# Kernel optimization log

Hardware: AMD Instinct MI355X
Metric: run time of the kernel (lower is better)

## Reference

```python
import jax, jax.numpy as jnp
import numpy as np

H = 16
D_MODEL = 1024
D_HID = 50  # hidden width of the 1->50->1 mask MLP


def setup_inputs() -> dict:
    key = jax.random.key(0)
    ks = jax.random.split(key, 16)
    B, S, D = 16, 768, D_MODEL
    n, nk = 512, 256  # code length n, redundancy n-k; S = n + nk
    inp = {
        "query": jax.random.normal(ks[0], (B, S, D), jnp.float32),
        "key": jax.random.normal(ks[1], (B, S, D), jnp.float32),
        "value": jax.random.normal(ks[2], (B, S, D), jnp.float32),
        "pc_matrix": jax.random.uniform(ks[3], (nk, n), jnp.float32),
        # four Linear(d_model, d_model) layers: q, k, v, out. Stored so that y = x @ W + b.
        "Wq": jax.random.normal(ks[4], (D, D), jnp.float32) * 0.02,
        "bq": jnp.zeros((D,), jnp.float32),
        "Wk": jax.random.normal(ks[5], (D, D), jnp.float32) * 0.02,
        "bk": jnp.zeros((D,), jnp.float32),
        "Wv": jax.random.normal(ks[6], (D, D), jnp.float32) * 0.02,
        "bv": jnp.zeros((D,), jnp.float32),
        "Wo": jax.random.normal(ks[7], (D, D), jnp.float32) * 0.02,
        "bo": jnp.zeros((D,), jnp.float32),
        # one_d_mapping: Linear(1,50) -> ReLU -> Linear(50,1)
        "mw1": jax.random.normal(ks[8], (1, D_HID), jnp.float32) * 0.5,
        "mb1": jax.random.normal(ks[9], (D_HID,), jnp.float32) * 0.1,
        "mw2": jax.random.normal(ks[10], (D_HID, 1), jnp.float32) * 0.5,
        "mb2": jnp.zeros((1,), jnp.float32),
    }
    return inp


def _mask_from_pc(pc, mw1, mb1, mw2, mb2):
    # pc: (nk, n). Build (S, S) block matrix, S = n + nk.
    nknk = pc @ pc.T            # (nk, nk)
    nn = pc.T @ pc              # (n, n)
    top = jnp.concatenate([nn, pc.T], axis=1)     # (n, S)
    bot = jnp.concatenate([pc, nknk], axis=1)     # (nk, S)
    M = jnp.concatenate([top, bot], axis=0)       # (S, S)
    # elementwise 1->50->1 MLP
    h = jax.nn.relu(M[..., None] * mw1[0] + mb1)  # (S, S, 50)
    out = h @ mw2 + mb2                           # (S, S, 1)
    return out[..., 0]                            # (S, S)


def reference(query, key, value, pc_matrix, Wq, bq, Wk, bk, Wv, bv, Wo, bo,
              mw1, mb1, mw2, mb2):
    B, S, D = query.shape
    dk = D // H
    q = (query @ Wq + bq).reshape(B, S, H, dk).transpose(0, 2, 1, 3)
    k = (key @ Wk + bk).reshape(B, S, H, dk).transpose(0, 2, 1, 3)
    v = (value @ Wv + bv).reshape(B, S, H, dk).transpose(0, 2, 1, 3)
    scores = jnp.einsum("bhqd,bhkd->bhqk", q, k) / jnp.sqrt(jnp.float32(dk))
    mask = _mask_from_pc(pc_matrix, mw1, mb1, mw2, mb2)  # (S, S)
    scores = scores * mask[None, None]  # multiplicative float mask
    p = jax.nn.softmax(scores, axis=-1)  # dropout is identity in eval mode
    x = jnp.einsum("bhqk,bhkd->bhqd", p, v)
    x = x.transpose(0, 2, 1, 3).reshape(B, S, D)
    return x @ Wo + bo
```

## Files before the change

kernel.cpp:

```cpp
#include <hip/hip_runtime.h>
#include <stdint.h>

typedef _Float16 f16;
typedef _Float16 f16x8 __attribute__((ext_vector_type(8)));
typedef float f32x4 __attribute__((ext_vector_type(4)));

union U4 { uint4 u; f16 h[8]; };
union U2 { uint2 u; f16 h[4]; };

#define GLOAD16(g, l)                                                         \
  __builtin_amdgcn_global_load_lds(                                           \
      (const __attribute__((address_space(1))) void*)(g),                     \
      (__attribute__((address_space(3))) void*)(l), 16, 0, 0)

__global__ __launch_bounds__(256) void k_wt(const float* __restrict__ W0,
                                            const float* __restrict__ W1,
                                            const float* __restrict__ W2,
                                            const float* __restrict__ W3,
                                            f16* __restrict__ T0, f16* __restrict__ T1,
                                            f16* __restrict__ T2, f16* __restrict__ T3) {
    __shared__ f16 tile[64 * 65];
    int z = blockIdx.z;
    const float* W = z == 0 ? W0 : z == 1 ? W1 : z == 2 ? W2 : W3;
    f16* Wt = z == 0 ? T0 : z == 1 ? T1 : z == 2 ? T2 : T3;
    int t = threadIdx.x;
    int k0 = blockIdx.x * 64, n0 = blockIdx.y * 64;
    #pragma unroll
    for (int i = 0; i < 4; i++) {
        int cid = t + i * 256;
        int row = cid >> 4, c4 = cid & 15;
        float4 v = *(const float4*)(W + (size_t)(k0 + row) * 1024 + n0 + c4 * 4);
        tile[(c4 * 4 + 0) * 65 + row] = (f16)v.x;
        tile[(c4 * 4 + 1) * 65 + row] = (f16)v.y;
        tile[(c4 * 4 + 2) * 65 + row] = (f16)v.z;
        tile[(c4 * 4 + 3) * 65 + row] = (f16)v.w;
    }
    __syncthreads();
    #pragma unroll
    for (int i = 0; i < 2; i++) {
        int cid = t + i * 256;
        int nr = cid >> 3, kc = cid & 7;
        U4 u;
        #pragma unroll
        for (int j = 0; j < 8; j++) u.h[j] = tile[nr * 65 + kc * 8 + j];
        *(uint4*)(Wt + (size_t)(n0 + nr) * 1024 + k0 + kc * 8) = u.u;
    }
}

__global__ __launch_bounds__(256) void k_cvt(const float* __restrict__ in,
                                             f16* __restrict__ out) {
    size_t id = (size_t)blockIdx.x * 256 + threadIdx.x;
    float4 a = *(const float4*)(in + id * 8);
    float4 b = *(const float4*)(in + id * 8 + 4);
    U4 u;
    u.h[0] = (f16)a.x; u.h[1] = (f16)a.y; u.h[2] = (f16)a.z; u.h[3] = (f16)a.w;
    u.h[4] = (f16)b.x; u.h[5] = (f16)b.y; u.h[6] = (f16)b.z; u.h[7] = (f16)b.w;
    *(uint4*)(out + id * 8) = u.u;
}

template <int TRANS>
__global__ __launch_bounds__(256) void k_gram(const float* __restrict__ pc,
                                              float* __restrict__ out) {
    constexpr int N = TRANS ? 256 : 512;
    constexpr int K = TRANS ? 512 : 256;
    __shared__ float As[16][68];
    __shared__ float Bs[16][68];
    int t = threadIdx.x;
    int i0 = blockIdx.x * 64, j0 = blockIdx.y * 64;
    int ty = t >> 4, tx = t & 15;
    float acc[4][4];
    #pragma unroll
    for (int r = 0; r < 4; r++)
        #pragma unroll
        for (int c = 0; c < 4; c++) acc[r][c] = 0.f;

    for (int kt = 0; kt < K; kt += 16) {
        if (TRANS == 0) {
            int k = t >> 4, c4 = t & 15;
            float4 va = *(const float4*)(pc + (size_t)(kt + k) * 512 + i0 + c4 * 4);
            float4 vb = *(const float4*)(pc + (size_t)(kt + k) * 512 + j0 + c4 * 4);
            *(float4*)&As[k][c4 * 4] = va;
            *(float4*)&Bs[k][c4 * 4] = vb;
        } else {
            int r = t >> 2, kc = t & 3;
            float4 va = *(const float4*)(pc + (size_t)(i0 + r) * 512 + kt + kc * 4);
            As[kc * 4 + 0][r] = va.x; As[kc * 4 + 1][r] = va.y;
            As[kc * 4 + 2][r] = va.z; As[kc * 4 + 3][r] = va.w;
            float4 vb = *(const float4*)(pc + (size_t)(j0 + r) * 512 + kt + kc * 4);
            Bs[kc * 4 + 0][r] = vb.x; Bs[kc * 4 + 1][r] = vb.y;
            Bs[kc * 4 + 2][r] = vb.z; Bs[kc * 4 + 3][r] = vb.w;
        }
        __syncthreads();
        #pragma unroll
        for (int u = 0; u < 16; u++) {
            float4 av = *(const float4*)&As[u][ty * 4];
            float4 bv = *(const float4*)&Bs[u][tx * 4];
            float aa[4] = {av.x, av.y, av.z, av.w};
            float bb[4] = {bv.x, bv.y, bv.z, bv.w};
            #pragma unroll
            for (int r = 0; r < 4; r++)
                #pragma unroll
                for (int c = 0; c < 4; c++) acc[r][c] += aa[r] * bb[c];
        }
        __syncthreads();
    }
    #pragma unroll
    for (int r = 0; r < 4; r++)
        #pragma unroll
        for (int c = 0; c < 4; c++)
            out[(size_t)(i0 + ty * 4 + r) * N + j0 + tx * 4 + c] = acc[r][c];
}

__global__ __launch_bounds__(256) void k_mask(const float* __restrict__ pc,
                                              const float* __restrict__ nn,
                                              const float* __restrict__ nknk,
                                              const float* __restrict__ mw1,
                                              const float* __restrict__ mb1,
                                              const float* __restrict__ mw2,
                                              const float* __restrict__ mb2,
                                              float* __restrict__ maskp) {
    __shared__ float w1[50], b1[50], w2[50];
    int t = threadIdx.x;
    if (t < 50) { w1[t] = mw1[t]; b1[t] = mb1[t]; w2[t] = mw2[t]; }
    __syncthreads();
    int id = blockIdx.x * 256 + t;
    int i = id / 768, j = id - i * 768;
    float M;
    if (i < 512) M = (j < 512) ? nn[(size_t)i * 512 + j] : pc[(size_t)(j - 512) * 512 + i];
    else         M = (j < 512) ? pc[(size_t)(i - 512) * 512 + j]
                               : nknk[(size_t)(i - 512) * 256 + (j - 512)];
    float acc = mb2[0];
    #pragma unroll 10
    for (int u = 0; u < 50; u++) acc += fmaxf(M * w1[u] + b1[u], 0.f) * w2[u];
    maskp[id] = acc * 0.18033688011112042f;
}

__global__ __launch_bounds__(256) void k_vt(const f16* __restrict__ Vh,
                                            f16* __restrict__ VT) {
    __shared__ f16 tile[64][72];
    int t = threadIdx.x;
    int s0 = blockIdx.x * 64;
    int bh = blockIdx.y, b = bh >> 4, h = bh & 15;
    #pragma unroll
    for (int p = 0; p < 2; p++) {
        int cid = t + p * 256;
        int s = cid >> 3, dc = cid & 7;
        *(uint4*)&tile[s][dc * 8] =
            *(const uint4*)(Vh + ((size_t)b * 768 + s0 + s) * 1024 + h * 64 + dc * 8);
    }
    __syncthreads();
    #pragma unroll
    for (int p = 0; p < 2; p++) {
        int cid = t + p * 256;
        int d = cid >> 3, sc = cid & 7;
        U4 u;
        #pragma unroll
        for (int j = 0; j < 8; j++) u.h[j] = tile[sc * 8 + j][d];
        *(uint4*)(VT + ((size_t)bh * 64 + d) * 768 + s0 + sc * 8) = u.u;
    }
}

template <int MODE>
__global__ __launch_bounds__(256) void k_gemm(const f16* __restrict__ A,
                                              const f16* __restrict__ Bt,
                                              const float* __restrict__ bias,
                                              void* out0v, void* out1v) {
    __shared__ f16 As[2][128 * 32];
    __shared__ f16 Bs[2][128 * 32];
    int t = threadIdx.x;
    int w = t >> 6, lane = t & 63, l15 = lane & 15, quad = lane >> 4;
    int wm = w >> 1, wn = w & 1;
    int id = blockIdx.x;
    int rest = id >> 3;
    int row0 = ((id & 7) * 12 + rest % 12) * 128;
    int n0 = (rest / 12) * 128;

    int m0 = w * 16 + (lane >> 2);
    int m1 = m0 + 64;
    int ks0 = (lane & 3) ^ ((m0 >> 1) & 3);
    int ks1 = (lane & 3) ^ ((m1 >> 1) & 3);
    const f16* gA0 = A + (size_t)(row0 + m0) * 1024 + ks0 * 8;
    const f16* gA1 = A + (size_t)(row0 + m1) * 1024 + ks1 * 8;
    const f16* gB0 = Bt + (size_t)(n0 + m0) * 1024 + ks0 * 8;
    const f16* gB1 = Bt + (size_t)(n0 + m1) * 1024 + ks1 * 8;
    int sw = (l15 >> 1) & 3;

    auto STAGE = [&](int bsel, int k0) {
        GLOAD16(gA0 + k0, &As[bsel][w * 512]);
        GLOAD16(gA1 + k0, &As[bsel][w * 512 + 2048]);
        GLOAD16(gB0 + k0, &Bs[bsel][w * 512]);
        GLOAD16(gB1 + k0, &Bs[bsel][w * 512 + 2048]);
    };

    f32x4 acc[4][4];
    #pragma unroll
    for (int mi = 0; mi < 4; mi++)
        #pragma unroll
        for (int ni = 0; ni < 4; ni++) acc[mi][ni] = (f32x4){0.f, 0.f, 0.f, 0.f};

    STAGE(0, 0);
    __syncthreads();
    int buf = 0;
    for (int kt = 0; kt < 32; kt++) {
        if (kt < 31) STAGE(buf ^ 1, (kt + 1) * 32);
        f16x8 af[4], bf_[4];
        #pragma unroll
        for (int mi = 0; mi < 4; mi++)
            af[mi] = *(const f16x8*)((const char*)&As[buf][0] +
                     (size_t)(wm * 64 + mi * 16 + l15) * 64 + ((quad ^ sw) << 4));
        #pragma unroll
        for (int ni = 0; ni < 4; ni++)
            bf_[ni] = *(const f16x8*)((const char*)&Bs[buf][0] +
                      (size_t)(wn * 64 + ni * 16 + l15) * 64 + ((quad ^ sw) << 4));
        #pragma unroll
        for (int mi = 0; mi < 4; mi++)
            #pragma unroll
            for (int ni = 0; ni < 4; ni++)
                acc[mi][ni] = __builtin_amdgcn_mfma_f32_16x16x32_f16(af[mi], bf_[ni],
                                                                     acc[mi][ni], 0, 0, 0);
        __syncthreads();
        buf ^= 1;
    }
    #pragma unroll
    for (int mi = 0; mi < 4; mi++) {
        #pragma unroll
        for (int ni = 0; ni < 4; ni++) {
            int col = n0 + wn * 64 + ni * 16 + l15;
            float bv = bias[col];
            #pragma unroll
            for (int r = 0; r < 4; r++) {
                int row = row0 + wm * 64 + mi * 16 + quad * 4 + r;
                float v = acc[mi][ni][r] + bv;
                size_t idx = (size_t)row * 1024 + col;
                if (MODE == 0) {
                    ((f16*)out0v)[idx] = (f16)v;
                } else if (MODE == 1) {
                    f16 hi = (f16)v;
                    ((f16*)out0v)[idx] = hi;
                    ((f16*)out1v)[idx] = (f16)(v - (float)hi);
                } else {
                    ((float*)out0v)[idx] = v;
                }
            }
        }
    }
}

__global__ __launch_bounds__(256) void k_attn(const f16* __restrict__ Qhi,
                                              const f16* __restrict__ Qlo,
                                              const f16* __restrict__ Khi,
                                              const f16* __restrict__ Klo,
                                              const f16* __restrict__ VT,
                                              const float* __restrict__ maskp,
                                              f16* __restrict__ Xout) {
    __shared__ f16 Ksh[2][64 * 64];
    __shared__ f16 Ksl[2][64 * 64];
    __shared__ f16 Vs[64 * 64];
    __shared__ f16 Ps[4][16 * 64];
    int t = threadIdx.x;
    int w = t >> 6, lane = t & 63, l15 = lane & 15, quad = lane >> 4;
    int id = blockIdx.x;
    int bh = (id & 7) + ((id >> 3) / 12) * 8;
    int q0 = ((id >> 3) % 12) * 64;
    int b = bh >> 4, h = bh & 15;
    const size_t base = ((size_t)b * 768) * 1024 + h * 64;

    int srow = lane >> 3;
    int sslot = lane & 7;

    f16x8 qh[2], ql[2];
    int qrow = q0 + w * 16 + l15;
    #pragma unroll
    for (int c = 0; c < 2; c++) {
        qh[c] = *(const f16x8*)(Qhi + base + (size_t)qrow * 1024 + c * 32 + quad * 8);
        ql[c] = *(const f16x8*)(Qlo + base + (size_t)qrow * 1024 + c * 32 + quad * 8);
    }
    float mrow = -1e30f, lrow = 0.f;
    f32x4 o[4];
    #pragma unroll
    for (int ni = 0; ni < 4; ni++) o[ni] = (f32x4){0.f, 0.f, 0.f, 0.f};

    auto STAGE_K = [&](int bsel, int k0) {
        #pragma unroll
        for (int p = 0; p < 2; p++) {
            int row = w * 16 + p * 8 + srow;
            int ss = sslot ^ (row & 7);
            GLOAD16(Khi + base + (size_t)(k0 + row) * 1024 + ss * 8,
                    &Ksh[bsel][w * 1024 + p * 512]);
            GLOAD16(Klo + base + (size_t)(k0 + row) * 1024 + ss * 8,
                    &Ksl[bsel][w * 1024 + p * 512]);
        }
    };
    auto STAGE_V = [&](int k0) {
        #pragma unroll
        for (int p = 0; p < 2; p++) {
            int row = w * 16 + p * 8 + srow;
            int ss = sslot ^ (row & 7);
            GLOAD16(VT + ((size_t)bh * 64 + row) * 768 + k0 + ss * 8,
                    &Vs[w * 1024 + p * 512]);
        }
    };

    STAGE_K(0, 0);
    asm volatile("s_waitcnt vmcnt(0)" ::: "memory");
    __builtin_amdgcn_s_barrier();
    int buf = 0;
    int kx = l15 & 7;
    const float* mbase = maskp + (size_t)quad * 4 * 768 + q0 + w * 16 + l15;

    for (int kt = 0; kt < 12; kt++) {
        int k0 = kt * 64;
        float mvs[4][4];
        #pragma unroll
        for (int kn = 0; kn < 4; kn++)
            #pragma unroll
            for (int r = 0; r < 4; r++)
                mvs[kn][r] = mbase[(size_t)(k0 + kn * 16 + r) * 768];
        STAGE_V(k0);
        if (kt < 11) STAGE_K(buf ^ 1, k0 + 64);

        float sv[4][4];
        #pragma unroll
        for (int kn = 0; kn < 4; kn++) {
            f32x4 s = (f32x4){0.f, 0.f, 0.f, 0.f};
            int key = kn * 16 + l15;
            #pragma unroll
            for (int c = 0; c < 2; c++) {
                int slot = ((c << 2) + quad) ^ kx;
                f16x8 kh = *(const f16x8*)((const char*)&Ksh[buf][0] +
                                           (size_t)key * 128 + (slot << 4));
                f16x8 kl = *(const f16x8*)((const char*)&Ksl[buf][0] +
                                           (size_t)key * 128 + (slot << 4));
                s = __builtin_amdgcn_mfma_f32_16x16x32_f16(kh, qh[c], s, 0, 0, 0);
                s = __builtin_amdgcn_mfma_f32_16x16x32_f16(kh, ql[c], s, 0, 0, 0);
                s = __builtin_amdgcn_mfma_f32_16x16x32_f16(kl, qh[c], s, 0, 0, 0);
            }
            #pragma unroll
            for (int r = 0; r < 4; r++) sv[kn][r] = s[r] * mvs[kn][r];
        }

        float g0 = fmaxf(fmaxf(sv[0][0], sv[0][1]), sv[0][2]);
        float g1 = fmaxf(fmaxf(sv[0][3], sv[1][0]), sv[1][1]);
        float g2 = fmaxf(fmaxf(sv[1][2], sv[1][3]), sv[2][0]);
        float g3 = fmaxf(fmaxf(sv[2][1], sv[2][2]), sv[2][3]);
        float g4 = fmaxf(fmaxf(sv[3][0], sv[3][1]), sv[3][2]);
        float tm = fmaxf(fmaxf(fmaxf(g0, g1), fmaxf(g2, g3)), fmaxf(g4, sv[3][3]));
        tm = fmaxf(tm, __shfl_xor(tm, 16));
        tm = fmaxf(tm, __shfl_xor(tm, 32));
        if (__any(tm > mrow + 11.0f)) {
            float mn = fmaxf(mrow, tm);
            float alpha = exp2f(mrow - mn);
            mrow = mn;
            lrow *= alpha;
            #pragma unroll
            for (int ni = 0; ni < 4; ni++)
                #pragma unroll
                for (int r = 0; r < 4; r++) o[ni][r] *= alpha;
        }
        float rs = 0.f;
        #pragma unroll
        for (int kn = 0; kn < 4; kn++) {
            U2 pk;
            #pragma unroll
            for (int r = 0; r < 4; r++) {
                float pv = exp2f(sv[kn][r] - mrow);
                rs += pv;
                pk.h[r] = (f16)pv;
            }
            int slot = (kn * 2 + (quad >> 1)) ^ kx;
            *(uint2*)((char*)&Ps[w][0] + l15 * 128 + (slot << 4) + ((quad & 1) << 3)) = pk.u;
        }
        rs += __shfl_xor(rs, 16);
        rs += __shfl_xor(rs, 32);
        lrow += rs;

        asm volatile("s_waitcnt lgkmcnt(0)" ::: "memory");
        if (kt < 11) asm volatile("s_waitcnt vmcnt(4)" ::: "memory");
        else         asm volatile("s_waitcnt vmcnt(0)" ::: "memory");
        __builtin_amdgcn_s_barrier();
        __builtin_amdgcn_sched_barrier(0);
        #pragma unroll
        for (int c = 0; c < 2; c++) {
            int pslot = ((c << 2) + quad) ^ kx;
            f16x8 pa = *(const f16x8*)((const char*)&Ps[w][0] +
                                       (size_t)l15 * 128 + (pslot << 4));
            #pragma unroll
            for (int ni = 0; ni < 4; ni++) {
                int d = ni * 16 + l15;
                f16x8 vb = *(const f16x8*)((const char*)&Vs[0] +
                                           (size_t)d * 128 + (pslot << 4));
                o[ni] = __builtin_amdgcn_mfma_f32_16x16x32_f16(vb, pa, o[ni], 0, 0, 0);
            }
        }
        asm volatile("s_waitcnt vmcnt(0)" ::: "memory");
        __builtin_amdgcn_s_barrier();
        buf ^= 1;
    }
    float rl = 1.0f / lrow;
    int qg = q0 + w * 16 + l15;
    #pragma unroll
    for (int ni = 0; ni < 4; ni++) {
        U2 ok;
        #pragma unroll
        for (int r = 0; r < 4; r++) ok.h[r] = (f16)(o[ni][r] * rl);
        *(uint2*)(Xout + ((size_t)b * 768 + qg) * 1024 + h * 64 + ni * 16 + quad * 4) = ok.u;
    }
}

extern "C" void kernel_launch(void* const* d_in, const int* in_sizes, int n_in,
                              void* d_out, int out_size, void* d_ws, size_t ws_size,
                              hipStream_t stream) {
    (void)in_sizes; (void)n_in; (void)out_size; (void)ws_size;
    const float* query = (const float*)d_in[0];
    const float* key   = (const float*)d_in[1];
    const float* value = (const float*)d_in[2];
    const float* pc    = (const float*)d_in[3];
    const float* Wq    = (const float*)d_in[4];
    const float* bq    = (const float*)d_in[5];
    const float* Wk    = (const float*)d_in[6];
    const float* bk    = (const float*)d_in[7];
    const float* Wv    = (const float*)d_in[8];
    const float* bv    = (const float*)d_in[9];
    const float* Wo    = (const float*)d_in[10];
    const float* bo    = (const float*)d_in[11];
    const float* mw1   = (const float*)d_in[12];
    const float* mb1   = (const float*)d_in[13];
    const float* mw2   = (const float*)d_in[14];
    const float* mb2   = (const float*)d_in[15];

    char* p = (char*)d_ws;
    auto take = [&](size_t bytes) -> char* {
        char* r = p; p += (bytes + 255) & ~(size_t)255; return r;
    };
    const size_t NTOK = 12288, DM = 1024;
    float* maskb = (float*)take(768 * 768 * 4);
    float* nnb   = (float*)take(512 * 512 * 4);
    float* nknkb = (float*)take(256 * 256 * 4);
    f16* Wqt = (f16*)take(DM * DM * 2);
    f16* Wkt = (f16*)take(DM * DM * 2);
    f16* Wvt = (f16*)take(DM * DM * 2);
    f16* Wot = (f16*)take(DM * DM * 2);
    f16* buf1 = (f16*)take(NTOK * DM * 2);
    f16* Qhi = (f16*)take(NTOK * DM * 2);
    f16* Qlo = (f16*)take(NTOK * DM * 2);
    f16* Khi = (f16*)take(NTOK * DM * 2);
    f16* Klo = (f16*)take(NTOK * DM * 2);
    f16* Vhb = (f16*)take(NTOK * DM * 2);
    f16* VTb = (f16*)take(NTOK * DM * 2);

    k_wt<<<dim3(16, 16, 4), 256, 0, stream>>>(Wq, Wk, Wv, Wo, Wqt, Wkt, Wvt, Wot);
    k_gram<0><<<dim3(8, 8), 256, 0, stream>>>(pc, nnb);
    k_gram<1><<<dim3(4, 4), 256, 0, stream>>>(pc, nknkb);
    k_mask<<<2304, 256, 0, stream>>>(pc, nnb, nknkb, mw1, mb1, mw2, mb2, maskb);

    k_cvt<<<6144, 256, 0, stream>>>(query, buf1);
    k_gemm<1><<<768, 256, 0, stream>>>(buf1, Wqt, bq, Qhi, Qlo);
    k_cvt<<<6144, 256, 0, stream>>>(key, buf1);
    k_gemm<1><<<768, 256, 0, stream>>>(buf1, Wkt, bk, Khi, Klo);
    k_cvt<<<6144, 256, 0, stream>>>(value, buf1);
    k_gemm<0><<<768, 256, 0, stream>>>(buf1, Wvt, bv, Vhb, nullptr);

    k_vt<<<dim3(12, 256), 256, 0, stream>>>(Vhb, VTb);

    k_attn<<<3072, 256, 0, stream>>>(Qhi, Qlo, Khi, Klo, VTb, maskb, buf1);

    k_gemm<2><<<768, 256, 0, stream>>>(buf1, Wot, bo, d_out, nullptr);
}
```

Before: 580.9 us.

## Replace 128x128 GEMM with 256x256-tile, 8-wave, BK=64 kernel

The projection GEMM goes from 128x128 tiles with 4 waves and K-step 32 to 256x256 tiles with 8 waves (512 threads) and K-step 64. Each wave now computes a 128x64 sub-tile, which raises operand reuse and cuts global and LDS traffic per flop. Staging uses an XOR swizzle on the 128-byte rows and issues the next loads right after the barrier, so there is one barrier per K-step. In exchange the grid shrinks to 192 blocks, which is fewer than the CU count, and LDS use (128 KB) and accumulator registers rise, lowering occupancy.

```diff
diff --git a/kernel.cpp b/kernel.cpp
--- a/kernel.cpp
+++ b/kernel.cpp
@@ -161,75 +161,93 @@
 }
 
 template <int MODE>
-__global__ __launch_bounds__(256) void k_gemm(const f16* __restrict__ A,
-                                              const f16* __restrict__ Bt,
-                                              const float* __restrict__ bias,
-                                              void* out0v, void* out1v) {
-    __shared__ f16 As[2][128 * 32];
-    __shared__ f16 Bs[2][128 * 32];
+__global__ __launch_bounds__(512) void k_gemm8(const f16* __restrict__ A,
+                                               const f16* __restrict__ Bt,
+                                               const float* __restrict__ bias,
+                                               void* out0v, void* out1v) {
+    __shared__ f16 Ab[2][2][128 * 64];
+    __shared__ f16 Bb[2][2][128 * 64];
     int t = threadIdx.x;
     int w = t >> 6, lane = t & 63, l15 = lane & 15, quad = lane >> 4;
-    int wm = w >> 1, wn = w & 1;
+    int wm = w >> 2, wn = w & 3;
     int id = blockIdx.x;
-    int rest = id >> 3;
-    int row0 = ((id & 7) * 12 + rest % 12) * 128;
-    int n0 = (rest / 12) * 128;
-
-    int m0 = w * 16 + (lane >> 2);
-    int m1 = m0 + 64;
-    int ks0 = (lane & 3) ^ ((m0 >> 1) & 3);
-    int ks1 = (lane & 3) ^ ((m1 >> 1) & 3);
-    const f16* gA0 = A + (size_t)(row0 + m0) * 1024 + ks0 * 8;
-    const f16* gA1 = A + (size_t)(row0 + m1) * 1024 + ks1 * 8;
-    const f16* gB0 = Bt + (size_t)(n0 + m0) * 1024 + ks0 * 8;
-    const f16* gB1 = Bt + (size_t)(n0 + m1) * 1024 + ks1 * 8;
-    int sw = (l15 >> 1) & 3;
-
-    auto STAGE = [&](int bsel, int k0) {
-        GLOAD16(gA0 + k0, &As[bsel][w * 512]);
-        GLOAD16(gA1 + k0, &As[bsel][w * 512 + 2048]);
-        GLOAD16(gB0 + k0, &Bs[bsel][w * 512]);
-        GLOAD16(gB1 + k0, &Bs[bsel][w * 512 + 2048]);
+    int c = id >> 3;
+    int row0 = ((id & 7) * 6 + c % 6) * 256;
+    int n0 = (c / 6) * 256;
+
+    int srow = lane >> 3;
+    int ss = (lane & 7) ^ srow;
+    const f16* gA = A + (size_t)(row0 + w * 8 + srow) * 1024 + ss * 8;
+    const f16* gB = Bt + (size_t)(n0 + w * 8 + srow) * 1024 + ss * 8;
+
+    auto STAGE = [&](int buf, int kt) {
+        #pragma unroll
+        for (int hf = 0; hf < 2; hf++)
+            #pragma unroll
+            for (int p = 0; p < 2; p++) {
+                size_t roff = (size_t)(hf * 128 + p * 64) * 1024 + kt * 64;
+                GLOAD16(gA + roff, &Ab[buf][hf][(p * 64 + w * 8) * 64]);
+                GLOAD16(gB + roff, &Bb[buf][hf][(p * 64 + w * 8) * 64]);
+            }
     };
 
-    f32x4 acc[4][4];
-    #pragma unroll
-    for (int mi = 0; mi < 4; mi++)
+    f32x4 acc[8][4];
+    #pragma unroll
+    for (int mi = 0; mi < 8; mi++)
         #pragma unroll
         for (int ni = 0; ni < 4; ni++) acc[mi][ni] = (f32x4){0.f, 0.f, 0.f, 0.f};
 
+    int rx = l15 & 7;
+
+    auto COMPUTE = [&](int buf) {
+        f16x8 bf[4][2];
+        #pragma unroll
+        for (int ni = 0; ni < 4; ni++) {
+            int row = wn * 64 + ni * 16 + l15;
+            const char* bb = (const char*)&Bb[buf][row >> 7][0] +
+                             (size_t)(row & 127) * 128;
+            #pragma unroll
+            for (int ks = 0; ks < 2; ks++)
+                bf[ni][ks] = *(const f16x8*)(bb + (((ks * 4 + quad) ^ rx) << 4));
+        }
+        #pragma unroll
+        for (int mi = 0; mi < 8; mi++) {
+            int row = wm * 128 + mi * 16 + l15;
+            const char* ab = (const char*)&Ab[buf][row >> 7][0] +
+                             (size_t)(row & 127) * 128;
+            f16x8 af0 = *(const f16x8*)(ab + (((0 + quad) ^ rx) << 4));
+            f16x8 af1 = *(const f16x8*)(ab + (((4 + quad) ^ rx) << 4));
+            #pragma unroll
+            for (int ni = 0; ni < 4; ni++) {
+                acc[mi][ni] = __builtin_amdgcn_mfma_f32_16x16x32_f16(af0, bf[ni][0],
+                                                                     acc[mi][ni], 0, 0, 0);
+                acc[mi][ni] = __builtin_amdgcn_mfma_f32_16x16x32_f16(af1, bf[ni][1],
+                                                                     acc[mi][ni], 0, 0, 0);
+            }
+        }
+    };
+
     STAGE(0, 0);
-    __syncthreads();
-    int buf = 0;
-    for (int kt = 0; kt < 32; kt++) {
-        if (kt < 31) STAGE(buf ^ 1, (kt + 1) * 32);
-        f16x8 af[4], bf_[4];
-        #pragma unroll
-        for (int mi = 0; mi < 4; mi++)
-            af[mi] = *(const f16x8*)((const char*)&As[buf][0] +
-                     (size_t)(wm * 64 + mi * 16 + l15) * 64 + ((quad ^ sw) << 4));
-        #pragma unroll
-        for (int ni = 0; ni < 4; ni++)
-            bf_[ni] = *(const f16x8*)((const char*)&Bs[buf][0] +
-                      (size_t)(wn * 64 + ni * 16 + l15) * 64 + ((quad ^ sw) << 4));
-        #pragma unroll
-        for (int mi = 0; mi < 4; mi++)
-            #pragma unroll
-            for (int ni = 0; ni < 4; ni++)
-                acc[mi][ni] = __builtin_amdgcn_mfma_f32_16x16x32_f16(af[mi], bf_[ni],
-                                                                     acc[mi][ni], 0, 0, 0);
-        __syncthreads();
-        buf ^= 1;
-    }
-    #pragma unroll
-    for (int mi = 0; mi < 4; mi++) {
+    asm volatile("s_waitcnt vmcnt(0)" ::: "memory");
+    __builtin_amdgcn_s_barrier();
+    STAGE(1, 1);
+    for (int kt = 0; kt < 16; kt++) {
+        int buf = kt & 1;
+        COMPUTE(buf);
+        asm volatile("s_waitcnt vmcnt(0)" ::: "memory");
+        __builtin_amdgcn_s_barrier();
+        if (kt + 2 < 16) STAGE(buf, kt + 2);
+    }
+
+    #pragma unroll
+    for (int mi = 0; mi < 8; mi++) {
         #pragma unroll
         for (int ni = 0; ni < 4; ni++) {
             int col = n0 + wn * 64 + ni * 16 + l15;
             float bv = bias[col];
             #pragma unroll
             for (int r = 0; r < 4; r++) {
-                int row = row0 + wm * 64 + mi * 16 + quad * 4 + r;
+                int row = row0 + wm * 128 + mi * 16 + quad * 4 + r;
                 float v = acc[mi][ni][r] + bv;
                 size_t idx = (size_t)row * 1024 + col;
                 if (MODE == 0) {
@@ -454,15 +472,15 @@
     k_mask<<<2304, 256, 0, stream>>>(pc, nnb, nknkb, mw1, mb1, mw2, mb2, maskb);
 
     k_cvt<<<6144, 256, 0, stream>>>(query, buf1);
-    k_gemm<1><<<768, 256, 0, stream>>>(buf1, Wqt, bq, Qhi, Qlo);
+    k_gemm8<1><<<192, 512, 0, stream>>>(buf1, Wqt, bq, Qhi, Qlo);
     k_cvt<<<6144, 256, 0, stream>>>(key, buf1);
-    k_gemm<1><<<768, 256, 0, stream>>>(buf1, Wkt, bk, Khi, Klo);
+    k_gemm8<1><<<192, 512, 0, stream>>>(buf1, Wkt, bk, Khi, Klo);
     k_cvt<<<6144, 256, 0, stream>>>(value, buf1);
-    k_gemm<0><<<768, 256, 0, stream>>>(buf1, Wvt, bv, Vhb, nullptr);
+    k_gemm8<0><<<192, 512, 0, stream>>>(buf1, Wvt, bv, Vhb, nullptr);
 
     k_vt<<<dim3(12, 256), 256, 0, stream>>>(Vhb, VTb);
 
     k_attn<<<3072, 256, 0, stream>>>(Qhi, Qlo, Khi, Klo, VTb, maskb, buf1);
 
-    k_gemm<2><<<768, 256, 0, stream>>>(buf1, Wot, bo, d_out, nullptr);
-}
+    k_gemm8<2><<<192, 512, 0, stream>>>(buf1, Wot, bo, d_out, nullptr);
+}
```

Measured after the change: 557.1 us. -4.1%, faster.
